# Performance work log

Hardware: AMD Instinct MI355X
Metric: run time of the kernel (lower is better)

Reference implementation:

```python
import jax, jax.numpy as jnp
import numpy as np
from jax import lax

NT, TL = 32, 64           # num_trajs, traj_length
H, W, C = 84, 84, 4       # Atari frame stack
SIZE = 256                # LSTM hidden size
NOUT = 18                 # num_outputs
FEAT = 6 * 6 * 32         # after four stride-2 SAME convs: 84->42->21->11->6
DN = ('NHWC', 'HWIO', 'NHWC')


def setup_inputs() -> dict:
    key = jax.random.key(0)
    ks = jax.random.split(key, 8)
    d = {}
    d['inputs'] = jax.random.normal(ks[0], (NT * TL, H, W, C), jnp.float32)
    cin = C
    for i in range(4):
        d[f'w{i+1}'] = jax.random.normal(ks[1 + i], (3, 3, cin, 32), jnp.float32) * 0.1
        d[f'b{i+1}'] = jnp.zeros((32,), jnp.float32)
        cin = 32
    d['lstm_w'] = jax.random.normal(ks[5], (FEAT + SIZE, 4 * SIZE), jnp.float32) * 0.05
    d['lstm_b'] = jnp.zeros((4 * SIZE,), jnp.float32)
    d['fc_w'] = jax.random.normal(ks[6], (SIZE, NOUT), jnp.float32) * 0.01
    d['fc_b'] = jnp.zeros((NOUT,), jnp.float32)
    d['c0'] = jnp.zeros((NT, SIZE), jnp.float32)
    d['h0'] = jnp.zeros((NT, SIZE), jnp.float32)
    return d


def reference(inputs, w1, b1, w2, b2, w3, b3, w4, b4,
              lstm_w, lstm_b, fc_w, fc_b, c0, h0):
    x = inputs
    for w, b in ((w1, b1), (w2, b2), (w3, b3), (w4, b4)):
        x = jax.nn.elu(lax.conv_general_dilated(
            x, w, window_strides=(2, 2), padding='SAME',
            dimension_numbers=DN) + b)
    # [NT*TL, 6, 6, 32] -> [TL, NT, FEAT] (time-major for scan)
    xs = x.reshape(NT, TL, FEAT).transpose(1, 0, 2)

    def step(carry, xt):
        c, h = carry
        gates = jnp.concatenate([xt, h], axis=-1) @ lstm_w + lstm_b
        i, j, f, o = jnp.split(gates, 4, axis=-1)
        # BasicLSTMCell with forget_bias = 1.0
        new_c = c * jax.nn.sigmoid(f + 1.0) + jax.nn.sigmoid(i) * jnp.tanh(j)
        new_h = jnp.tanh(new_c) * jax.nn.sigmoid(o)
        return (new_c, new_h), new_h

    _, outs = lax.scan(step, (c0, h0), xs)          # outs: [TL, NT, SIZE]
    feats = outs.transpose(1, 0, 2).reshape(-1, SIZE)  # batch-major flatten
    logits = feats @ fc_w + fc_b                    # [NT*TL, NOUT]
    return logits
```

## Files before the change

kernel.cpp:

```cpp
#include <hip/hip_runtime.h>
#include <math.h>

#define NTRAJ 32
#define TLEN  64
#define BATCH (NTRAJ*TLEN)

__device__ __forceinline__ float eluf(float x){ return x > 0.f ? x : expm1f(x); }
__device__ __forceinline__ float sigmf(float x){ return 1.f/(1.f+expf(-x)); }

__global__ __launch_bounds__(256) void conv1_kernel(
    const float* __restrict__ in,
    const float* __restrict__ w,
    const float* __restrict__ b,
    float* __restrict__ out)
{
    int bid = blockIdx.x;
    bid = (bid & 7)*1764 + (bid >> 3);
    int pos = bid*256 + threadIdx.x;
    int n   = pos / (42*42);
    int rem = pos % (42*42);
    int oy  = rem / 42, ox = rem % 42;
    float acc[32];
    #pragma unroll
    for(int o=0;o<32;o++) acc[o] = b[o];
    for(int ky=0; ky<3; ky++){
        int iy = 2*oy + ky;
        if(iy >= 84) continue;
        for(int kx=0; kx<3; kx++){
            int ix = 2*ox + kx;
            if(ix >= 84) continue;
            float4 v = *(const float4*)(in + (((n*84 + iy)*84) + ix)*4);
            const float* wq = w + (ky*3 + kx)*128;
            #pragma unroll
            for(int o=0;o<32;o++) acc[o] += v.x*wq[o];
            #pragma unroll
            for(int o=0;o<32;o++) acc[o] += v.y*wq[32+o];
            #pragma unroll
            for(int o=0;o<32;o++) acc[o] += v.z*wq[64+o];
            #pragma unroll
            for(int o=0;o<32;o++) acc[o] += v.w*wq[96+o];
        }
    }
    float4* op = (float4*)(out + (size_t)pos*32);
    #pragma unroll
    for(int q=0;q<8;q++)
        op[q] = make_float4(eluf(acc[4*q]), eluf(acc[4*q+1]),
                            eluf(acc[4*q+2]), eluf(acc[4*q+3]));
}

template<int IH, int IW, int OH, int OW, int PB>
__global__ __launch_bounds__(256) void convN_kernel(
    const float* __restrict__ in,
    const float* __restrict__ w,
    const float* __restrict__ b,
    float* __restrict__ out)
{
    int bid = blockIdx.x;
    const int cpx = gridDim.x >> 3;
    bid = (bid & 7)*cpx + (bid >> 3);
    int pos = bid*256 + threadIdx.x;
    if(pos >= BATCH*OH*OW) return;
    int n   = pos / (OH*OW);
    int rem = pos % (OH*OW);
    int oy  = rem / OW, ox = rem % OW;
    float acc[32];
    #pragma unroll
    for(int o=0;o<32;o++) acc[o] = b[o];
    for(int ky=0; ky<3; ky++){
        int iy = 2*oy + ky - PB;
        if(iy < 0 || iy >= IH) continue;
        for(int kx=0; kx<3; kx++){
            int ix = 2*ox + kx - PB;
            if(ix < 0 || ix >= IW) continue;
            const float4* ip = (const float4*)(in + ((size_t)(n*IH + iy)*IW + ix)*32);
            const float* wp = w + (ky*3 + kx)*1024;
            #pragma unroll
            for(int c4=0;c4<8;c4++){
                float4 x = ip[c4];
                const float* wq = wp + c4*128;
                #pragma unroll
                for(int o=0;o<32;o++) acc[o] += x.x*wq[o];
                #pragma unroll
                for(int o=0;o<32;o++) acc[o] += x.y*wq[32+o];
                #pragma unroll
                for(int o=0;o<32;o++) acc[o] += x.z*wq[64+o];
                #pragma unroll
                for(int o=0;o<32;o++) acc[o] += x.w*wq[96+o];
            }
        }
    }
    float4* op = (float4*)(out + (size_t)pos*32);
    #pragma unroll
    for(int q=0;q<8;q++)
        op[q] = make_float4(eluf(acc[4*q]), eluf(acc[4*q+1]),
                            eluf(acc[4*q+2]), eluf(acc[4*q+3]));
}

__global__ __launch_bounds__(256) void relayout_kernel(
    const float* __restrict__ p4,
    float* __restrict__ at)
{
    int i = blockIdx.x*256 + threadIdx.x;
    int f = i >> 11, r = i & 2047;
    int tt = r >> 5, n = r & 31;
    int nt = n*64 + tt;
    at[i] = p4[nt*1152 + f];
}

__global__ __launch_bounds__(256) void gx_gemm_kernel(
    const float* __restrict__ at,
    const float* __restrict__ lw,
    const float* __restrict__ lb,
    float* __restrict__ gx,
    unsigned int* __restrict__ bar)
{
    if(blockIdx.x == 0 && blockIdx.y == 0 && threadIdx.x < 128)
        bar[threadIdx.x*32] = 0u;
    int lane = threadIdx.x & 63;
    int wv   = threadIdx.x >> 6;
    int r0   = blockIdx.x * 16;
    int oc   = blockIdx.y*256 + wv*64 + lane;
    float acc[16];
    float bias = lb[oc];
    #pragma unroll
    for(int i=0;i<16;i++) acc[i] = bias;
    #pragma unroll 4
    for(int k=0;k<1152;k++){
        float wval = lw[k*1024 + oc];
        const float* ap = at + k*2048 + r0;
        #pragma unroll
        for(int i=0;i<16;i++) acc[i] += ap[i] * wval;
    }
    #pragma unroll
    for(int i=0;i<16;i++) gx[(r0+i)*1024 + oc] = acc[i];
}

__global__ __launch_bounds__(256) void lstm_coop_kernel(
    const float* __restrict__ gx,
    const float* __restrict__ lw,
    const float* __restrict__ c0,
    const float* __restrict__ h0,
    float* __restrict__ feats,
    float* __restrict__ hbuf,
    unsigned int* __restrict__ bar)
{
    __shared__ float hs[32*260];
    __shared__ float wl[8*260];
    __shared__ float gl[32*9];

    const int wg = blockIdx.x;
    const int t  = threadIdx.x;
    const int n    = t >> 3;
    const int cidx = t & 7;
    const int gcol = (cidx>>1)*256 + wg*2 + (cidx&1);
    const float* wh = lw + 1152*1024;

    #pragma unroll
    for(int i=0;i<8;i++){
        int e = t + 256*i;
        int k = e >> 3, cc = e & 7;
        int gc = (cc>>1)*256 + wg*2 + (cc&1);
        wl[cc*260 + k] = wh[k*1024 + gc];
    }
    const int un = t >> 1, uu = t & 1;
    float cst = (t < 64) ? c0[un*256 + wg*2 + uu] : 0.f;

    float4* hs4 = (float4*)hs;

    for(int st=0; st<64; ++st){
        const float4* hp4 = (const float4*)((st == 0) ? h0 : (hbuf + ((st&1)^1)*8192));
        #pragma unroll
        for(int i=0;i<8;i++){
            int q = t + 256*i;
            int row = q >> 6, col4 = q & 63;
            hs4[row*65 + col4] = hp4[q];
        }
        float gxv = gx[(st*32 + n)*1024 + gcol];
        __syncthreads();
        float a = 0.f;
        const float4* hr = (const float4*)&hs[n*260];
        const float4* wr = (const float4*)&wl[cidx*260];
        #pragma unroll 8
        for(int k4=0;k4<64;k4++){
            float4 hv = hr[k4];
            float4 wv = wr[k4];
            a += hv.x*wv.x + hv.y*wv.y + hv.z*wv.z + hv.w*wv.w;
        }
        gl[n*9 + cidx] = a + gxv;
        __syncthreads();
        if(t < 64){
            float i_ = gl[un*9 +     uu];
            float j_ = gl[un*9 + 2 + uu];
            float f_ = gl[un*9 + 4 + uu];
            float o_ = gl[un*9 + 6 + uu];
            cst = cst*sigmf(f_ + 1.f) + sigmf(i_)*tanhf(j_);
            float h = tanhf(cst)*sigmf(o_);
            int col = wg*2 + uu;
            hbuf[(st&1)*8192 + un*256 + col] = h;
            feats[(un*64 + st)*256 + col]    = h;
        }
        if(st != 63){
            __syncthreads();
            if(t == 0)
                __hip_atomic_store(bar + wg*32, (unsigned)(st+1),
                                   __ATOMIC_RELEASE, __HIP_MEMORY_SCOPE_AGENT);
            if(t < 128){
                unsigned tgt = (unsigned)(st+1);
                unsigned spins = 0;
                while(__hip_atomic_load(bar + t*32, __ATOMIC_ACQUIRE,
                                        __HIP_MEMORY_SCOPE_AGENT) < tgt){
                    __builtin_amdgcn_s_sleep(1);
                    if(++spins > 20000000u) break;
                }
            }
            __syncthreads();
        }
    }
}

__global__ __launch_bounds__(64) void fc_kernel(
    const float* __restrict__ feats, const float* __restrict__ fw,
    const float* __restrict__ fb,    float* __restrict__ out)
{
    __shared__ float h[256];
    int p = blockIdx.x, t = threadIdx.x;
    *(float4*)&h[t*4] = *(const float4*)(feats + p*256 + t*4);
    __syncthreads();
    if(t < 18){
        float acc = fb[t];
        for(int k=0;k<256;k++) acc += h[k]*fw[k*18 + t];
        out[p*18 + t] = acc;
    }
}

extern "C" void kernel_launch(void* const* d_in, const int* in_sizes, int n_in,
                              void* d_out, int out_size, void* d_ws, size_t ws_size,
                              hipStream_t stream) {
    const float* inp = (const float*)d_in[0];
    const float* w1  = (const float*)d_in[1];  const float* b1 = (const float*)d_in[2];
    const float* w2  = (const float*)d_in[3];  const float* b2 = (const float*)d_in[4];
    const float* w3  = (const float*)d_in[5];  const float* b3 = (const float*)d_in[6];
    const float* w4  = (const float*)d_in[7];  const float* b4 = (const float*)d_in[8];
    const float* lw  = (const float*)d_in[9];  const float* lb = (const float*)d_in[10];
    const float* fw  = (const float*)d_in[11]; const float* fb = (const float*)d_in[12];
    const float* c0  = (const float*)d_in[13]; const float* h0 = (const float*)d_in[14];
    float* out = (float*)d_out;
    float* ws  = (float*)d_ws;

    const size_t n1 = (size_t)32*3612672;
    const size_t n3 = (size_t)32*247808;
    const size_t n4 = (size_t)32*73728;

    float* p1 = ws;
    float* p2 = p1 + n1;
    float* p3 = ws;
    float* p4 = p3 + n3;
    float* at = p4 + n4;
    float* gxb   = at  + (size_t)1152*2048;
    float* feats = gxb + (size_t)2048*1024;
    float* hbuf  = feats + (size_t)2048*256;
    unsigned int* bar = (unsigned int*)(hbuf + 2*32*256);

    conv1_kernel<<<14112,256,0,stream>>>(inp, w1, b1, p1);
    convN_kernel<42,42,21,21,0><<<3528,256,0,stream>>>(p1, w2, b2, p2);
    convN_kernel<21,21,11,11,1><<<968,256,0,stream>>>(p2, w3, b3, p3);
    convN_kernel<11,11, 6, 6,1><<<288,256,0,stream>>>(p3, w4, b4, p4);
    relayout_kernel<<<9216,256,0,stream>>>(p4, at);
    gx_gemm_kernel<<<dim3(128,4),256,0,stream>>>(at, lw, lb, gxb, bar);
    lstm_coop_kernel<<<128,256,0,stream>>>(gxb, lw, c0, h0, feats, hbuf, bar);
    fc_kernel<<<2048,64,0,stream>>>(feats, fw, fb, out);
}
```

Measured before the change: 2.019 ms.

## Replace LSTM grid barrier with tagged per-step h flags and fewer blocks

The recurrent LSTM kernel drops from 128 to 32 blocks, each owning 8 hidden units (32 gate columns), and computes a 2x2 register tile per thread. The global barrier (flag store plus 128-thread spin) is replaced by packing each h value with its step number into a 64-bit word in a per-step buffer, which consumers poll directly. This is meant to remove barrier round-trip latency and the extra syncthreads from each of the 64 serial steps. In exchange it needs a 64-step history buffer that must be zeroed each call (done in the relayout kernel), and each element load may spin.

```diff
diff --git a/kernel.cpp b/kernel.cpp
--- a/kernel.cpp
+++ b/kernel.cpp
@@ -98,9 +98,11 @@
 
 __global__ __launch_bounds__(256) void relayout_kernel(
     const float* __restrict__ p4,
-    float* __restrict__ at)
+    float* __restrict__ at,
+    unsigned long long* __restrict__ hbuf)
 {
     int i = blockIdx.x*256 + threadIdx.x;
+    if(i < 64*8192) hbuf[i] = 0ull;
     int f = i >> 11, r = i & 2047;
     int tt = r >> 5, n = r & 31;
     int nt = n*64 + tt;
@@ -111,11 +113,8 @@
     const float* __restrict__ at,
     const float* __restrict__ lw,
     const float* __restrict__ lb,
-    float* __restrict__ gx,
-    unsigned int* __restrict__ bar)
-{
-    if(blockIdx.x == 0 && blockIdx.y == 0 && threadIdx.x < 128)
-        bar[threadIdx.x*32] = 0u;
+    float* __restrict__ gx)
+{
     int lane = threadIdx.x & 63;
     int wv   = threadIdx.x >> 6;
     int r0   = blockIdx.x * 16;
@@ -141,80 +140,104 @@
     const float* __restrict__ c0,
     const float* __restrict__ h0,
     float* __restrict__ feats,
-    float* __restrict__ hbuf,
-    unsigned int* __restrict__ bar)
+    unsigned long long* __restrict__ hbuf)
 {
     __shared__ float hs[32*260];
-    __shared__ float wl[8*260];
-    __shared__ float gl[32*9];
+    __shared__ float wp[16*516];
+    __shared__ float gl[32*33];
 
     const int wg = blockIdx.x;
     const int t  = threadIdx.x;
-    const int n    = t >> 3;
-    const int cidx = t & 7;
-    const int gcol = (cidx>>1)*256 + wg*2 + (cidx&1);
     const float* wh = lw + 1152*1024;
 
-    #pragma unroll
-    for(int i=0;i<8;i++){
+    for(int i=0;i<32;i++){
         int e = t + 256*i;
-        int k = e >> 3, cc = e & 7;
-        int gc = (cc>>1)*256 + wg*2 + (cc&1);
-        wl[cc*260 + k] = wh[k*1024 + gc];
-    }
-    const int un = t >> 1, uu = t & 1;
-    float cst = (t < 64) ? c0[un*256 + wg*2 + uu] : 0.f;
-
-    float4* hs4 = (float4*)hs;
+        int k = e >> 5, c = e & 31;
+        int gc = (c>>3)*256 + wg*8 + (c&7);
+        wp[(c>>1)*516 + (k>>1)*4 + (k&1)*2 + (c&1)] = wh[k*1024 + gc];
+    }
+    const int un = t >> 3, uu = t & 7;
+    float cst = c0[un*256 + wg*8 + uu];
+
+    const int np = t >> 4, cp = t & 15;
+    const int n0 = 2*np, n1 = 2*np + 1;
+    const int c0l = 2*cp, c1l = 2*cp + 1;
+    const int g0 = (c0l>>3)*256 + wg*8 + (c0l&7);
+    const int g1 = (c1l>>3)*256 + wg*8 + (c1l&7);
+
+    const float4* hs4 = (const float4*)hs;
+    const float4* wp4 = (const float4*)wp;
+    __syncthreads();
 
     for(int st=0; st<64; ++st){
-        const float4* hp4 = (const float4*)((st == 0) ? h0 : (hbuf + ((st&1)^1)*8192));
-        #pragma unroll
-        for(int i=0;i<8;i++){
-            int q = t + 256*i;
-            int row = q >> 6, col4 = q & 63;
-            hs4[row*65 + col4] = hp4[q];
-        }
-        float gxv = gx[(st*32 + n)*1024 + gcol];
+        const float* gr0 = gx + (size_t)(st*32 + n0)*1024;
+        const float* gr1 = gx + (size_t)(st*32 + n1)*1024;
+        float gx00 = gr0[g0], gx01 = gr0[g1];
+        float gx10 = gr1[g0], gx11 = gr1[g1];
+
+        if(st == 0){
+            const float4* hp4 = (const float4*)h0;
+            #pragma unroll
+            for(int i=0;i<8;i++){
+                int q = t + 256*i;
+                int row = q >> 6, col4 = q & 63;
+                ((float4*)hs)[row*65 + col4] = hp4[q];
+            }
+        } else {
+            const unsigned long long* src = hbuf + (size_t)(st-1)*8192;
+            const unsigned tag = (unsigned)st;
+            #pragma unroll
+            for(int i=0;i<32;i++){
+                int q = i*256 + t;
+                unsigned long long v = __hip_atomic_load(&src[q],
+                    __ATOMIC_RELAXED, __HIP_MEMORY_SCOPE_AGENT);
+                unsigned spins = 0;
+                while((unsigned)(v >> 32) != tag){
+                    __builtin_amdgcn_s_sleep(1);
+                    v = __hip_atomic_load(&src[q],
+                        __ATOMIC_RELAXED, __HIP_MEMORY_SCOPE_AGENT);
+                    if(++spins > (1u<<23)) break;
+                }
+                hs[i*260 + t] = __uint_as_float((unsigned)v);
+            }
+        }
         __syncthreads();
-        float a = 0.f;
-        const float4* hr = (const float4*)&hs[n*260];
-        const float4* wr = (const float4*)&wl[cidx*260];
+
+        float a00=0.f, a01=0.f, a10=0.f, a11=0.f;
+        const float4* h0r = hs4 + n0*65;
+        const float4* h1r = hs4 + n1*65;
+        const float4* wr  = wp4 + cp*129;
         #pragma unroll 8
         for(int k4=0;k4<64;k4++){
-            float4 hv = hr[k4];
-            float4 wv = wr[k4];
-            a += hv.x*wv.x + hv.y*wv.y + hv.z*wv.z + hv.w*wv.w;
-        }
-        gl[n*9 + cidx] = a + gxv;
+            float4 A = wr[2*k4], B = wr[2*k4+1];
+            float4 x = h0r[k4], y = h1r[k4];
+            a00 += x.x*A.x + x.y*A.z + x.z*B.x + x.w*B.z;
+            a01 += x.x*A.y + x.y*A.w + x.z*B.y + x.w*B.w;
+            a10 += y.x*A.x + y.y*A.z + y.z*B.x + y.w*B.z;
+            a11 += y.x*A.y + y.y*A.w + y.z*B.y + y.w*B.w;
+        }
+        gl[n0*33 + c0l] = a00 + gx00;
+        gl[n0*33 + c1l] = a01 + gx01;
+        gl[n1*33 + c0l] = a10 + gx10;
+        gl[n1*33 + c1l] = a11 + gx11;
         __syncthreads();
-        if(t < 64){
-            float i_ = gl[un*9 +     uu];
-            float j_ = gl[un*9 + 2 + uu];
-            float f_ = gl[un*9 + 4 + uu];
-            float o_ = gl[un*9 + 6 + uu];
+
+        {
+            float i_ = gl[un*33 +      uu];
+            float j_ = gl[un*33 +  8 + uu];
+            float f_ = gl[un*33 + 16 + uu];
+            float o_ = gl[un*33 + 24 + uu];
             cst = cst*sigmf(f_ + 1.f) + sigmf(i_)*tanhf(j_);
             float h = tanhf(cst)*sigmf(o_);
-            int col = wg*2 + uu;
-            hbuf[(st&1)*8192 + un*256 + col] = h;
-            feats[(un*64 + st)*256 + col]    = h;
-        }
-        if(st != 63){
-            __syncthreads();
-            if(t == 0)
-                __hip_atomic_store(bar + wg*32, (unsigned)(st+1),
-                                   __ATOMIC_RELEASE, __HIP_MEMORY_SCOPE_AGENT);
-            if(t < 128){
-                unsigned tgt = (unsigned)(st+1);
-                unsigned spins = 0;
-                while(__hip_atomic_load(bar + t*32, __ATOMIC_ACQUIRE,
-                                        __HIP_MEMORY_SCOPE_AGENT) < tgt){
-                    __builtin_amdgcn_s_sleep(1);
-                    if(++spins > 20000000u) break;
-                }
-            }
-            __syncthreads();
-        }
+            int col = wg*8 + uu;
+            feats[(un*64 + st)*256 + col] = h;
+            unsigned long long pv =
+                ((unsigned long long)(unsigned)(st+1) << 32) |
+                (unsigned long long)__float_as_uint(h);
+            __hip_atomic_store(&hbuf[(size_t)st*8192 + un*256 + col], pv,
+                               __ATOMIC_RELAXED, __HIP_MEMORY_SCOPE_AGENT);
+        }
+        __syncthreads();
     }
 }
 
@@ -258,15 +281,15 @@
     float* at = p4 + n4;
     float* gxb   = at  + (size_t)1152*2048;
     float* feats = gxb + (size_t)2048*1024;
-    float* hbuf  = feats + (size_t)2048*256;
-    unsigned int* bar = (unsigned int*)(hbuf + 2*32*256);
+    unsigned long long* hbuf =
+        (unsigned long long*)(feats + (size_t)2048*256);
 
     conv1_kernel<<<14112,256,0,stream>>>(inp, w1, b1, p1);
     convN_kernel<42,42,21,21,0><<<3528,256,0,stream>>>(p1, w2, b2, p2);
     convN_kernel<21,21,11,11,1><<<968,256,0,stream>>>(p2, w3, b3, p3);
     convN_kernel<11,11, 6, 6,1><<<288,256,0,stream>>>(p3, w4, b4, p4);
-    relayout_kernel<<<9216,256,0,stream>>>(p4, at);
-    gx_gemm_kernel<<<dim3(128,4),256,0,stream>>>(at, lw, lb, gxb, bar);
-    lstm_coop_kernel<<<128,256,0,stream>>>(gxb, lw, c0, h0, feats, hbuf, bar);
+    relayout_kernel<<<9216,256,0,stream>>>(p4, at, hbuf);
+    gx_gemm_kernel<<<dim3(128,4),256,0,stream>>>(at, lw, lb, gxb);
+    lstm_coop_kernel<<<32,256,0,stream>>>(gxb, lw, c0, h0, feats, hbuf);
     fc_kernel<<<2048,64,0,stream>>>(feats, fw, fb, out);
 }
```

Measured after the change: 2.238 ms. 10.8% more time.
